# Kernel tuning notes

Measured on AMD Instinct MI355X. Metric: run time of the kernel, lower is better.

The kernel has to match this reference:

```python
import jax, jax.numpy as jnp
import numpy as np

BATCH, N_REC, D_HIDDEN = 8192, 1024, 2048
RMIN, RMAX = 0.4, 0.99

def _half_glorot(key, shape):
    # VarianceScaling(scale=1/2, fan_avg, uniform): limit = sqrt(3*scale/fan_avg)
    fan_avg = (shape[0] + shape[1]) / 2.0
    limit = np.sqrt(1.5 / fan_avg)
    return jax.random.uniform(key, shape, jnp.float32, -limit, limit)

def setup_inputs() -> dict:
    key = jax.random.key(0)
    ks = jax.random.split(key, 11)
    inputs = jax.random.normal(ks[0], (BATCH, N_REC), jnp.float32)
    state_re = jax.random.normal(ks[1], (BATCH, D_HIDDEN), jnp.float32)
    state_im = jax.random.normal(ks[2], (BATCH, D_HIDDEN), jnp.float32)
    C_re = _half_glorot(ks[3], (D_HIDDEN, N_REC))
    C_im = _half_glorot(ks[4], (D_HIDDEN, N_REC))
    B_re = _half_glorot(ks[5], (N_REC, D_HIDDEN))
    B_im = _half_glorot(ks[6], (N_REC, D_HIDDEN))
    D = jax.random.normal(ks[7], (N_REC,), jnp.float32)
    numax = float(np.log(-np.log(RMIN)))
    numin = float(np.log(-np.log(RMAX)))
    nu = jax.random.uniform(ks[8], (D_HIDDEN,), jnp.float32, numin, numax)
    theta = jax.random.uniform(ks[9], (D_HIDDEN,), jnp.float32, 0.0, 3.14 / 10)
    # gamma initialized to sqrt(1 - |lambda|^2), |lambda| = exp(-exp(nu))
    gamma = jnp.sqrt(1.0 - jnp.exp(-2.0 * jnp.exp(nu)))
    return {"inputs": inputs, "state_re": state_re, "state_im": state_im,
            "B_re": B_re, "B_im": B_im, "C_re": C_re, "C_im": C_im,
            "D": D, "nu": nu, "theta": theta, "gamma": gamma}

def reference(inputs, state_re, state_im, B_re, B_im, C_re, C_im, D, nu, theta, gamma):
    # lambda = exp(-exp(nu) + i*theta), diagonal complex recurrence
    lam = (jnp.exp(-jnp.exp(nu)) * jnp.exp(1j * theta)).astype(jnp.complex64)  # [H]
    x = (state_re + 1j * state_im).astype(jnp.complex64)  # [B,H]
    B = (B_re + 1j * B_im).astype(jnp.complex64)          # [N,H]
    C = (C_re + 1j * C_im).astype(jnp.complex64)          # [H,N]
    u_ = inputs.astype(jnp.complex64)
    new_u = gamma.astype(jnp.complex64) * (u_ @ B)        # [B,H]
    x_ = x * lam + new_u                                  # diag matmul == elementwise
    y = jnp.real(x_ @ C) + D * inputs                     # [B,N]
    return y, jnp.real(x_), jnp.imag(x_)
```

## Files before the change

### kernel.cpp

```cpp
#include <hip/hip_runtime.h>
#include <hip/hip_bf16.h>

typedef __bf16 bf16;
typedef __attribute__((ext_vector_type(8))) __bf16 bf16x8;
typedef __attribute__((ext_vector_type(4))) float floatx4;

#define BATCH 8192
#define NREC  1024
#define DHID  2048

#define GLOBAL_AS __attribute__((address_space(1)))
#define LDS_AS    __attribute__((address_space(3)))

__device__ __forceinline__ bf16 to_bf16(float f) { return (bf16)f; }

__device__ __forceinline__ void async16(const void* g, void* l) {
  __builtin_amdgcn_global_load_lds((const GLOBAL_AS unsigned int*)g,
                                   (LDS_AS unsigned int*)l, 16, 0, 0);
}

__device__ __forceinline__ bf16x8 ldsFrag(const bf16* buf, int row, int q) {
  const int s = (q ^ ((row >> 1) & 3)) * 8;
  return *reinterpret_cast<const bf16x8*>(&buf[row * 32 + s]);
}


__global__ void lam_kernel(const float* __restrict__ nu, const float* __restrict__ theta,
                           float* __restrict__ lamRe, float* __restrict__ lamIm) {
  int h = blockIdx.x * blockDim.x + threadIdx.x;
  if (h < DHID) {
    float t = expf(-expf(nu[h]));
    lamRe[h] = t * cosf(theta[h]);
    lamIm[h] = t * sinf(theta[h]);
  }
}

__global__ void convert_kernel(const float* __restrict__ src, bf16* __restrict__ dst) {
  int idx = blockIdx.x * blockDim.x + threadIdx.x;
  float4 v = reinterpret_cast<const float4*>(src)[idx];
  ushort4 pk;
  pk.x = __builtin_bit_cast(unsigned short, to_bf16(v.x));
  pk.y = __builtin_bit_cast(unsigned short, to_bf16(v.y));
  pk.z = __builtin_bit_cast(unsigned short, to_bf16(v.z));
  pk.w = __builtin_bit_cast(unsigned short, to_bf16(v.w));
  *reinterpret_cast<ushort4*>(dst + (size_t)idx * 4) = pk;
}

__global__ void transpose_kernel(const float* __restrict__ src, int C,
                                 bf16* __restrict__ dst, int dstStride, float scale) {
  __shared__ float tile[32][33];
  int c0 = blockIdx.x * 32, r0 = blockIdx.y * 32;
  #pragma unroll
  for (int i = 0; i < 32; i += 8) {
    tile[threadIdx.y + i][threadIdx.x] =
        src[(size_t)(r0 + threadIdx.y + i) * C + c0 + threadIdx.x];
  }
  __syncthreads();
  #pragma unroll
  for (int i = 0; i < 32; i += 8) {
    int c = c0 + threadIdx.y + i;
    dst[(size_t)c * dstStride + r0 + threadIdx.x] =
        to_bf16(scale * tile[threadIdx.x][threadIdx.y + i]);
  }
}


__global__ __launch_bounds__(512, 3) void gemm1_kernel(
    const bf16* __restrict__ A,
    const bf16* __restrict__ BreT,
    const bf16* __restrict__ BimT,
    const float* __restrict__ state_re,
    const float* __restrict__ state_im,
    const float* __restrict__ gamma,
    const float* __restrict__ lamRe,
    const float* __restrict__ lamIm,
    float* __restrict__ xre_out,
    float* __restrict__ xim_out,
    bf16* __restrict__ Xcat)
{
  __shared__ __align__(16) bf16 Alds[2][128 * 32];
  __shared__ __align__(16) bf16 BreLds[2][128 * 32];
  __shared__ __align__(16) bf16 BimLds[2][128 * 32];

  const int tid   = threadIdx.x;
  const int mBase = blockIdx.y * 128;
  const int hBase = blockIdx.x * 128;
  const int lane  = tid & 63;
  const int wave  = tid >> 6;
  const int wr    = (wave >> 2) * 64;
  const int wc    = (wave & 3) * 32;
  const int m16   = lane & 15;
  const int q     = lane >> 4;

  floatx4 zero = {0.f, 0.f, 0.f, 0.f};
  floatx4 accRe[4][2], accIm[4][2];
  #pragma unroll
  for (int i = 0; i < 4; ++i)
    #pragma unroll
    for (int j = 0; j < 2; ++j) { accRe[i][j] = zero; accIm[i][j] = zero; }

  const int row0 = tid >> 2;
  const int ss   = ((tid & 3) ^ ((row0 >> 1) & 3)) * 8;
  const int wbase = wave * 512;

  auto stage = [&](int buf, int kt) {
    const size_t aoff = (size_t)(mBase + row0) * 1024 + kt + ss;
    const size_t boff = (size_t)(hBase + row0) * 1024 + kt + ss;
    async16(&A[aoff],    &Alds[buf][wbase]);
    async16(&BreT[boff], &BreLds[buf][wbase]);
    async16(&BimT[boff], &BimLds[buf][wbase]);
  };

  auto computeTile = [&](int buf) {
    bf16x8 aF[4], brF[2], biF[2];
    #pragma unroll
    for (int i = 0; i < 4; ++i)
      aF[i] = ldsFrag(Alds[buf], wr + i * 16 + m16, q);
    #pragma unroll
    for (int j = 0; j < 2; ++j) {
      brF[j] = ldsFrag(BreLds[buf], wc + j * 16 + m16, q);
      biF[j] = ldsFrag(BimLds[buf], wc + j * 16 + m16, q);
    }
    #pragma unroll
    for (int i = 0; i < 4; ++i)
      #pragma unroll
      for (int j = 0; j < 2; ++j) {
        accRe[i][j] = __builtin_amdgcn_mfma_f32_16x16x32_bf16(aF[i], brF[j], accRe[i][j], 0, 0, 0);
        accIm[i][j] = __builtin_amdgcn_mfma_f32_16x16x32_bf16(aF[i], biF[j], accIm[i][j], 0, 0, 0);
      }
  };

  stage(0, 0);
  __syncthreads();
  int cur = 0;
  for (int kt = 32; kt < 1024; kt += 32) {
    stage(cur ^ 1, kt);
    computeTile(cur);
    __syncthreads();
    cur ^= 1;
  }
  computeTile(cur);

  #pragma unroll
  for (int j = 0; j < 2; ++j) {
    const int h  = hBase + wc + j * 16 + m16;
    const float g  = gamma[h];
    const float lr = lamRe[h];
    const float li = lamIm[h];
    #pragma unroll
    for (int i = 0; i < 4; ++i) {
      #pragma unroll
      for (int r = 0; r < 4; ++r) {
        const int row = mBase + wr + i * 16 + q * 4 + r;
        const size_t off = (size_t)row * DHID + h;
        const float ur = g * accRe[i][j][r];
        const float ui = g * accIm[i][j][r];
        const float sr = state_re[off];
        const float si = state_im[off];
        const float xr = sr * lr - si * li + ur;
        const float xi = sr * li + si * lr + ui;
        xre_out[off] = xr;
        xim_out[off] = xi;
        const size_t xoff = (size_t)row * (2 * DHID) + h;
        Xcat[xoff]        = to_bf16(xr);
        Xcat[xoff + DHID] = to_bf16(xi);
      }
    }
  }
}


__global__ __launch_bounds__(512, 4) void gemm2_kernel(
    const bf16* __restrict__ Xcat,
    const bf16* __restrict__ CcatT,
    const float* __restrict__ Dvec,
    const float* __restrict__ inputs,
    float* __restrict__ y)
{
  __shared__ __align__(16) bf16 Alds[2][128 * 32];
  __shared__ __align__(16) bf16 Blds[2][128 * 32];

  const int tid   = threadIdx.x;
  const int mBase = blockIdx.y * 128;
  const int nBase = blockIdx.x * 128;
  const int lane  = tid & 63;
  const int wave  = tid >> 6;
  const int wr    = (wave >> 2) * 64;
  const int wc    = (wave & 3) * 32;
  const int m16   = lane & 15;
  const int q     = lane >> 4;

  floatx4 zero = {0.f, 0.f, 0.f, 0.f};
  floatx4 acc[4][2];
  #pragma unroll
  for (int i = 0; i < 4; ++i)
    #pragma unroll
    for (int j = 0; j < 2; ++j) acc[i][j] = zero;

  const int row0 = tid >> 2;
  const int ss   = ((tid & 3) ^ ((row0 >> 1) & 3)) * 8;
  const int wbase = wave * 512;

  auto stage = [&](int buf, int kt) {
    const size_t aoff = (size_t)(mBase + row0) * 4096 + kt + ss;
    const size_t boff = (size_t)(nBase + row0) * 4096 + kt + ss;
    async16(&Xcat[aoff],  &Alds[buf][wbase]);
    async16(&CcatT[boff], &Blds[buf][wbase]);
  };

  auto computeTile = [&](int buf) {
    bf16x8 aF[4], bF[2];
    #pragma unroll
    for (int i = 0; i < 4; ++i)
      aF[i] = ldsFrag(Alds[buf], wr + i * 16 + m16, q);
    #pragma unroll
    for (int j = 0; j < 2; ++j)
      bF[j] = ldsFrag(Blds[buf], wc + j * 16 + m16, q);
    #pragma unroll
    for (int i = 0; i < 4; ++i)
      #pragma unroll
      for (int j = 0; j < 2; ++j)
        acc[i][j] = __builtin_amdgcn_mfma_f32_16x16x32_bf16(aF[i], bF[j], acc[i][j], 0, 0, 0);
  };

  stage(0, 0);
  __syncthreads();
  int cur = 0;
  for (int kt = 32; kt < 4096; kt += 32) {
    stage(cur ^ 1, kt);
    computeTile(cur);
    __syncthreads();
    cur ^= 1;
  }
  computeTile(cur);

  #pragma unroll
  for (int j = 0; j < 2; ++j) {
    const int n = nBase + wc + j * 16 + m16;
    const float dv = Dvec[n];
    #pragma unroll
    for (int i = 0; i < 4; ++i) {
      #pragma unroll
      for (int r = 0; r < 4; ++r) {
        const int row = mBase + wr + i * 16 + q * 4 + r;
        const size_t idx = (size_t)row * NREC + n;
        y[idx] = acc[i][j][r] + dv * inputs[idx];
      }
    }
  }
}


extern "C" void kernel_launch(void* const* d_in, const int* in_sizes, int n_in,
                              void* d_out, int out_size, void* d_ws, size_t ws_size,
                              hipStream_t stream) {
  (void)in_sizes; (void)n_in; (void)out_size; (void)ws_size;

  const float* inputs   = (const float*)d_in[0];
  const float* state_re = (const float*)d_in[1];
  const float* state_im = (const float*)d_in[2];
  const float* B_re     = (const float*)d_in[3];
  const float* B_im     = (const float*)d_in[4];
  const float* C_re     = (const float*)d_in[5];
  const float* C_im     = (const float*)d_in[6];
  const float* Dvec     = (const float*)d_in[7];
  const float* nu       = (const float*)d_in[8];
  const float* theta    = (const float*)d_in[9];
  const float* gamma    = (const float*)d_in[10];

  float* out     = (float*)d_out;
  float* y_out   = out;
  float* xre_out = out + (size_t)BATCH * NREC;
  float* xim_out = xre_out + (size_t)BATCH * DHID;

  char* ws = (char*)d_ws;
  bf16*  A1    = (bf16*)(ws + 0);
  bf16*  BreT  = (bf16*)(ws + 16777216);
  bf16*  BimT  = (bf16*)(ws + 20971520);
  bf16*  CcatT = (bf16*)(ws + 25165824);
  bf16*  Xcat  = (bf16*)(ws + 33554432);
  float* lamRe = (float*)(ws + 100663296);
  float* lamIm = (float*)(ws + 100671488);

  lam_kernel<<<dim3(DHID / 256), dim3(256), 0, stream>>>(nu, theta, lamRe, lamIm);
  convert_kernel<<<dim3((BATCH * NREC) / 1024), dim3(256), 0, stream>>>(inputs, A1);

  dim3 tb(32, 8);
  transpose_kernel<<<dim3(2048 / 32, 1024 / 32), tb, 0, stream>>>(B_re, 2048, BreT, 1024, 1.0f);
  transpose_kernel<<<dim3(2048 / 32, 1024 / 32), tb, 0, stream>>>(B_im, 2048, BimT, 1024, 1.0f);
  transpose_kernel<<<dim3(1024 / 32, 2048 / 32), tb, 0, stream>>>(C_re, 1024, CcatT, 4096, 1.0f);
  transpose_kernel<<<dim3(1024 / 32, 2048 / 32), tb, 0, stream>>>(C_im, 1024, CcatT + 2048, 4096, -1.0f);

  gemm1_kernel<<<dim3(DHID / 128, BATCH / 128), dim3(512), 0, stream>>>(
      A1, BreT, BimT, state_re, state_im, gamma, lamRe, lamIm, xre_out, xim_out, Xcat);

  gemm2_kernel<<<dim3(NREC / 128, BATCH / 128), dim3(512), 0, stream>>>(
      Xcat, CcatT, Dvec, inputs, y_out);
}
```

Before: 565.6 us.

## Merge prep kernels into one launch and remap GEMM tiles across XCDs

Combines the lambda, input-conversion and four transpose kernels into a single prep kernel whose blocks dispatch on block index, cutting five launches and their serialization gaps. Both GEMM kernels now remap the linear block id so that consecutive logical tiles land on the same XCD (assuming round-robin dispatch over 8 XCDs), which is meant to improve L2 reuse of shared A/B panels. The prep kernel has a __syncthreads inside a branch that is uniform per block, so it is safe. The remap assumes the total block count is divisible by 8.

After: 554.7 us. Within noise of the previous version (-1.9%).

```diff
diff --git a/kernel.cpp b/kernel.cpp
--- a/kernel.cpp
+++ b/kernel.cpp
@@ -24,43 +24,57 @@
   return *reinterpret_cast<const bf16x8*>(&buf[row * 32 + s]);
 }
 
-
-__global__ void lam_kernel(const float* __restrict__ nu, const float* __restrict__ theta,
-                           float* __restrict__ lamRe, float* __restrict__ lamIm) {
-  int h = blockIdx.x * blockDim.x + threadIdx.x;
+__global__ __launch_bounds__(256) void prep_kernel(
+    const float* __restrict__ inputs, bf16* __restrict__ A1,
+    const float* __restrict__ B_re, const float* __restrict__ B_im,
+    bf16* __restrict__ BreT, bf16* __restrict__ BimT,
+    const float* __restrict__ C_re, const float* __restrict__ C_im,
+    bf16* __restrict__ CcatT,
+    const float* __restrict__ nu, const float* __restrict__ theta,
+    float* __restrict__ lamRe, float* __restrict__ lamIm)
+{
+  __shared__ float tile[32][33];
+  const int b   = blockIdx.x;
+  const int tid = threadIdx.x;
+
+  if (b < 8192) {
+    const int idx = b * 256 + tid;
+    float4 v = reinterpret_cast<const float4*>(inputs)[idx];
+    ushort4 pk;
+    pk.x = __builtin_bit_cast(unsigned short, to_bf16(v.x));
+    pk.y = __builtin_bit_cast(unsigned short, to_bf16(v.y));
+    pk.z = __builtin_bit_cast(unsigned short, to_bf16(v.z));
+    pk.w = __builtin_bit_cast(unsigned short, to_bf16(v.w));
+    *reinterpret_cast<ushort4*>(A1 + (size_t)idx * 4) = pk;
+    return;
+  }
+  if (b < 16384) {
+    const float* src; bf16* dst; int C, dstStride; float scale; int t;
+    if (b < 10240)      { t = b - 8192;  src = B_re; dst = BreT;         C = 2048; dstStride = 1024; scale =  1.0f; }
+    else if (b < 12288) { t = b - 10240; src = B_im; dst = BimT;         C = 2048; dstStride = 1024; scale =  1.0f; }
+    else if (b < 14336) { t = b - 12288; src = C_re; dst = CcatT;        C = 1024; dstStride = 4096; scale =  1.0f; }
+    else                { t = b - 14336; src = C_im; dst = CcatT + 2048; C = 1024; dstStride = 4096; scale = -1.0f; }
+    const int gx = C / 32;
+    const int bx = t % gx, by = t / gx;
+    const int c0 = bx * 32, r0 = by * 32;
+    const int tx = tid & 31, ty = tid >> 5;
+    #pragma unroll
+    for (int i = 0; i < 32; i += 8) {
+      tile[ty + i][tx] = src[(size_t)(r0 + ty + i) * C + c0 + tx];
+    }
+    __syncthreads();
+    #pragma unroll
+    for (int i = 0; i < 32; i += 8) {
+      const int c = c0 + ty + i;
+      dst[(size_t)c * dstStride + r0 + tx] = to_bf16(scale * tile[tx][ty + i]);
+    }
+    return;
+  }
+  const int h = (b - 16384) * 256 + tid;
   if (h < DHID) {
-    float t = expf(-expf(nu[h]));
-    lamRe[h] = t * cosf(theta[h]);
-    lamIm[h] = t * sinf(theta[h]);
-  }
-}
-
-__global__ void convert_kernel(const float* __restrict__ src, bf16* __restrict__ dst) {
-  int idx = blockIdx.x * blockDim.x + threadIdx.x;
-  float4 v = reinterpret_cast<const float4*>(src)[idx];
-  ushort4 pk;
-  pk.x = __builtin_bit_cast(unsigned short, to_bf16(v.x));
-  pk.y = __builtin_bit_cast(unsigned short, to_bf16(v.y));
-  pk.z = __builtin_bit_cast(unsigned short, to_bf16(v.z));
-  pk.w = __builtin_bit_cast(unsigned short, to_bf16(v.w));
-  *reinterpret_cast<ushort4*>(dst + (size_t)idx * 4) = pk;
-}
-
-__global__ void transpose_kernel(const float* __restrict__ src, int C,
-                                 bf16* __restrict__ dst, int dstStride, float scale) {
-  __shared__ float tile[32][33];
-  int c0 = blockIdx.x * 32, r0 = blockIdx.y * 32;
-  #pragma unroll
-  for (int i = 0; i < 32; i += 8) {
-    tile[threadIdx.y + i][threadIdx.x] =
-        src[(size_t)(r0 + threadIdx.y + i) * C + c0 + threadIdx.x];
-  }
-  __syncthreads();
-  #pragma unroll
-  for (int i = 0; i < 32; i += 8) {
-    int c = c0 + threadIdx.y + i;
-    dst[(size_t)c * dstStride + r0 + threadIdx.x] =
-        to_bf16(scale * tile[threadIdx.x][threadIdx.y + i]);
+    float tt = expf(-expf(nu[h]));
+    lamRe[h] = tt * cosf(theta[h]);
+    lamIm[h] = tt * sinf(theta[h]);
   }
 }
 
@@ -82,9 +96,13 @@
   __shared__ __align__(16) bf16 BreLds[2][128 * 32];
   __shared__ __align__(16) bf16 BimLds[2][128 * 32];
 
-  const int tid   = threadIdx.x;
-  const int mBase = blockIdx.y * 128;
-  const int hBase = blockIdx.x * 128;
+  const int tid = threadIdx.x;
+  const int d       = blockIdx.x + blockIdx.y * gridDim.x;
+  const int cpx     = (gridDim.x * gridDim.y) >> 3;
+  const int logical = (d & 7) * cpx + (d >> 3);
+  const int mBase = (logical / gridDim.x) * 128;
+  const int hBase = (logical % gridDim.x) * 128;
+
   const int lane  = tid & 63;
   const int wave  = tid >> 6;
   const int wr    = (wave >> 2) * 64;
@@ -180,9 +198,13 @@
   __shared__ __align__(16) bf16 Alds[2][128 * 32];
   __shared__ __align__(16) bf16 Blds[2][128 * 32];
 
-  const int tid   = threadIdx.x;
-  const int mBase = blockIdx.y * 128;
-  const int nBase = blockIdx.x * 128;
+  const int tid = threadIdx.x;
+  const int d       = blockIdx.x + blockIdx.y * gridDim.x;
+  const int cpx     = (gridDim.x * gridDim.y) >> 3;
+  const int logical = (d & 7) * cpx + (d >> 3);
+  const int mBase = (logical / gridDim.x) * 128;
+  const int nBase = (logical % gridDim.x) * 128;
+
   const int lane  = tid & 63;
   const int wave  = tid >> 6;
   const int wr    = (wave >> 2) * 64;
@@ -282,14 +304,9 @@
   float* lamRe = (float*)(ws + 100663296);
   float* lamIm = (float*)(ws + 100671488);
 
-  lam_kernel<<<dim3(DHID / 256), dim3(256), 0, stream>>>(nu, theta, lamRe, lamIm);
-  convert_kernel<<<dim3((BATCH * NREC) / 1024), dim3(256), 0, stream>>>(inputs, A1);
-
-  dim3 tb(32, 8);
-  transpose_kernel<<<dim3(2048 / 32, 1024 / 32), tb, 0, stream>>>(B_re, 2048, BreT, 1024, 1.0f);
-  transpose_kernel<<<dim3(2048 / 32, 1024 / 32), tb, 0, stream>>>(B_im, 2048, BimT, 1024, 1.0f);
-  transpose_kernel<<<dim3(1024 / 32, 2048 / 32), tb, 0, stream>>>(C_re, 1024, CcatT, 4096, 1.0f);
-  transpose_kernel<<<dim3(1024 / 32, 2048 / 32), tb, 0, stream>>>(C_im, 1024, CcatT + 2048, 4096, -1.0f);
+  prep_kernel<<<dim3(16392), dim3(256), 0, stream>>>(
+      inputs, A1, B_re, B_im, BreT, BimT, C_re, C_im, CcatT,
+      nu, theta, lamRe, lamIm);
 
   gemm1_kernel<<<dim3(DHID / 128, BATCH / 128), dim3(512), 0, stream>>>(
       A1, BreT, BimT, state_re, state_im, gamma, lamRe, lamIm, xre_out, xim_out, Xcat);
```
